# Kernel tuning notes

Hardware: AMD Instinct MI355X
Metric: run time of the kernel (lower is better)

## Reference

```python
import jax, jax.numpy as jnp
import numpy as np

GRID_MIN, GRID_MAX = -3.0, 3.0
N_AXIS = 64            # 64x64 grid -> m = 4096
LENGTHSCALE = 0.5      # RBF kernel lengthscale
EPS = 1e-6


def make_grid():
    lin = jnp.linspace(GRID_MIN, GRID_MAX, N_AXIS, dtype=jnp.float32)
    gx, gy = jnp.meshgrid(lin, lin, indexing='ij')
    return jnp.stack([gx.ravel(), gy.ravel()], axis=-1)  # [m, 2]


def setup_inputs() -> dict:
    key = jax.random.key(0)
    k1, k2 = jax.random.split(key)
    X = jax.random.normal(k1, (16, 1024, 2), dtype=jnp.float32)  # context locations
    Y = jax.random.normal(k2, (16, 1024, 8), dtype=jnp.float32)  # context values
    return {"X": X, "Y": Y}


def reference(X, Y):
    grid = make_grid()                                   # [m, 2]
    # expand_with_ones: prepend a ones channel (density channel)
    ones = jnp.ones(Y.shape[:-1] + (1,), dtype=Y.dtype)
    Yb = jnp.concatenate([ones, Y], axis=-1)             # [b, n, 1+dy]

    # kernel_smooth: RBF kernel between grid and X, contracted with Yb.
    # squared distances via the expanded form (avoids [b,m,n,2] intermediate)
    g2 = jnp.sum(grid * grid, axis=-1)                   # [m]
    x2 = jnp.sum(X * X, axis=-1)                         # [b, n]
    gx = jnp.einsum('md,bnd->bmn', grid, X)              # [b, m, n]
    d2 = g2[None, :, None] + x2[:, None, :] - 2.0 * gx   # [b, m, n]
    K = jnp.exp(-d2 / (2.0 * LENGTHSCALE * LENGTHSCALE)) # [b, m, n]

    Y_grid = jnp.einsum('bmn,bnc->bmc', K, Yb)           # [b, m, 1+dy]

    # normalise: divide feature channels by the density channel
    density = Y_grid[:, :, :1]
    feats = Y_grid[:, :, 1:] / (density + EPS)
    Y_grid = jnp.concatenate([density, feats], axis=-1)

    return grid[None], Y_grid
```

## Files before the change

### kernel.cpp

```cpp
#include <hip/hip_runtime.h>

typedef _Float16 half8   __attribute__((ext_vector_type(8)));
typedef float    floatx4 __attribute__((ext_vector_type(4)));

#define STEP  (6.0f / 63.0f)
#define SCAL  1.69864636f

__global__ __launch_bounds__(512, 2) void rkhs_fused(
    const float* __restrict__ X,
    const float* __restrict__ Y,
    float* __restrict__ out)
{
    __shared__ __align__(16) unsigned char smem[65536];
    float2*   sX    = (float2*)smem;
    float*    sYf   = (float*)(smem + 2048);
    _Float16* sEx   = (_Float16*)(smem + 10240);
    _Float16* sYb   = (_Float16*)(smem + 12288);
    _Float16* sEy   = (_Float16*)(smem + 20480);
    floatx4*  spark = (floatx4*)smem;
    float*    sfin  = (float*)smem;

    const int b   = blockIdx.x >> 4;
    const int rw  = blockIdx.x & 15;
    const int tid = threadIdx.x;
    const int w   = tid >> 6, l = tid & 63, q = l >> 4, n = l & 15;
    const int r0  = rw * 4;

    if (b == 0) {
        const int row = r0 + (tid >> 7), rem = tid & 127;
        out[(size_t)rw * 512 + tid] = (rem & 1)
            ? (-3.0f + (float)(rem >> 1) * STEP)
            : (-3.0f + (float)row * STEP);
    }

    floatx4 acc[4][4];
#pragma unroll
    for (int rr = 0; rr < 4; ++rr)
#pragma unroll
        for (int ct = 0; ct < 4; ++ct) acc[rr][ct] = (floatx4){0.f, 0.f, 0.f, 0.f};

    for (int c = 0; c < 4; ++c) {
        const int kb = c * 256;
        __syncthreads();
        if (tid < 256)
            sX[tid] = ((const float2*)X)[b * 1024 + kb + tid];
        ((float4*)sYf)[tid] =
            ((const float4*)(Y + ((size_t)b * 1024 + kb) * 8))[tid];
        __syncthreads();

        if (tid < 128) {
            const int s_loc = tid >> 4, rr = (tid >> 2) & 3, qq = tid & 3;
            const int kk = s_loc * 32 + qq * 8;
            const float gS = SCAL * (-3.0f + (float)(r0 + rr) * STEP);
            half8 h;
#pragma unroll
            for (int j = 0; j < 8; ++j) {
                const float d = fmaf(-SCAL, sX[kk + j].x, gS);
                h[j] = (_Float16)__builtin_amdgcn_exp2f(-(d * d));
            }
            *(half8*)(sEx + (s_loc * 4 + rr) * 32 + qq * 8) = h;
        }
        {
            const int kk = w * 32 + q * 8;
            half8 h;
#pragma unroll
            for (int j = 0; j < 8; ++j) {
                float v = 0.f;
                if (n == 0)      v = 1.f;
                else if (n <= 8) v = sYf[(kk + j) * 8 + n - 1];
                h[j] = (_Float16)v;
            }
            *(half8*)(sYb + (w * 64 + l) * 8) = h;
        }
#pragma unroll
        for (int i = 0; i < 4; ++i) {
            const int u = tid + 512 * i;
            const int ll = u & 63;
            const int kk = ((u >> 8) & 7) * 32 + (ll >> 4) * 8;
            const int col = ((u >> 6) & 3) * 16 + (ll & 15);
            const float gS = SCAL * (-3.0f + (float)col * STEP);
            half8 h;
#pragma unroll
            for (int j = 0; j < 8; ++j) {
                const float d = fmaf(-SCAL, sX[kk + j].y, gS);
                h[j] = (_Float16)__builtin_amdgcn_exp2f(-(d * d));
            }
            *(half8*)(sEy + (size_t)u * 8) = h;
        }
        __syncthreads();

        {
            const half8 yb = *(const half8*)(sYb + (w * 64 + l) * 8);
            half8 bp[4];
#pragma unroll
            for (int rr = 0; rr < 4; ++rr)
                bp[rr] = (*(const half8*)(sEx + (w * 4 + rr) * 32 + q * 8)) * yb;
#pragma unroll
            for (int ct = 0; ct < 4; ++ct) {
                const half8 ey = *(const half8*)(sEy + ((w * 4 + ct) * 64 + l) * 8);
#pragma unroll
                for (int rr = 0; rr < 4; ++rr)
                    acc[rr][ct] = __builtin_amdgcn_mfma_f32_16x16x32_f16(ey, bp[rr], acc[rr][ct], 0, 0, 0);
            }
        }
    }
    __syncthreads();

#define PARKA(slot)                                                        \
    { _Pragma("unroll") for (int rr = 0; rr < 4; ++rr)                     \
      _Pragma("unroll") for (int ct = 0; ct < 4; ++ct)                     \
          spark[(slot) * 1024 + (rr * 4 + ct) * 64 + l] = acc[rr][ct]; }
#define ABSORBA(slot)                                                      \
    { _Pragma("unroll") for (int rr = 0; rr < 4; ++rr)                     \
      _Pragma("unroll") for (int ct = 0; ct < 4; ++ct)                     \
          acc[rr][ct] += spark[(slot) * 1024 + (rr * 4 + ct) * 64 + l]; }

    if (w >= 4) PARKA(w - 4)
    __syncthreads();
    if (w < 4)  ABSORBA(w)
    __syncthreads();
    if (w == 2 || w == 3) PARKA(w - 2)
    __syncthreads();
    if (w < 2)  ABSORBA(w)
    __syncthreads();
    if (w == 1) PARKA(0)
    __syncthreads();

    if (w == 0) {
        ABSORBA(0)
#pragma unroll
        for (int rr = 0; rr < 4; ++rr)
#pragma unroll
            for (int ct = 0; ct < 4; ++ct)
                if (n < 9)
#pragma unroll
                    for (int i = 0; i < 4; ++i)
                        sfin[(rr * 64 + ct * 16 + q * 4 + i) * 9 + n] = acc[rr][ct][i];
    }
#undef PARKA
#undef ABSORBA
    __syncthreads();

    const size_t obase = 8192 + ((size_t)b * 4096 + (size_t)r0 * 64) * 9;
#pragma unroll
    for (int it = 0; it < 5; ++it) {
        const int idx = it * 512 + tid;
        if (idx < 2304) {
            const int m  = idx / 9;
            const int ch = idx - m * 9;
            const float dens = sfin[m * 9];
            const float v    = sfin[idx];
            out[obase + idx] = ch ? v * __builtin_amdgcn_rcpf(dens + 1e-6f) : dens;
        }
    }
}

extern "C" void kernel_launch(void* const* d_in, const int* in_sizes, int n_in,
                              void* d_out, int out_size, void* d_ws, size_t ws_size,
                              hipStream_t stream) {
    const float* X = (const float*)d_in[0];
    const float* Y = (const float*)d_in[1];
    float* out = (float*)d_out;

    rkhs_fused<<<dim3(256), dim3(512), 0, stream>>>(X, Y, out);
}
```

Measured before the change: 65.98 us.

## Stage whole context once and compute y-exponentials in registers

Replaces the four-chunk loop, which had two barriers per chunk and staged Y and the y-axis exponential tile through shared memory, with one up-front staging step and a single barrier. Each wave now loads its Y fragments straight from global memory into registers. The x-axis exponentials for all 1024 points are precomputed into shared memory once. The y-axis exponentials are computed in registers right before each MFMA instead of being stored and reloaded from LDS. This cuts synchronization and LDS traffic, but adds register pressure and moves the exp work into the MFMA loop.

```diff
diff --git a/kernel.cpp b/kernel.cpp
--- a/kernel.cpp
+++ b/kernel.cpp
@@ -12,11 +12,8 @@
     float* __restrict__ out)
 {
     __shared__ __align__(16) unsigned char smem[65536];
-    float2*   sX    = (float2*)smem;
-    float*    sYf   = (float*)(smem + 2048);
-    _Float16* sEx   = (_Float16*)(smem + 10240);
-    _Float16* sYb   = (_Float16*)(smem + 12288);
-    _Float16* sEy   = (_Float16*)(smem + 20480);
+    float*    sXy   = (float*)smem;
+    _Float16* sEx   = (_Float16*)(smem + 4096);
     floatx4*  spark = (floatx4*)smem;
     float*    sfin  = (float*)smem;
 
@@ -26,6 +23,13 @@
     const int w   = tid >> 6, l = tid & 63, q = l >> 4, n = l & 15;
     const int r0  = rw * 4;
 
+    {
+        const float2 v0 = ((const float2*)X)[b * 1024 + 2 * tid];
+        const float2 v1 = ((const float2*)X)[b * 1024 + 2 * tid + 1];
+        sXy[2 * tid]     = SCAL * v0.y;
+        sXy[2 * tid + 1] = SCAL * v1.y;
+    }
+
     if (b == 0) {
         const int row = r0 + (tid >> 7), rem = tid & 127;
         out[(size_t)rw * 512 + tid] = (rem & 1)
@@ -33,75 +37,76 @@
             : (-3.0f + (float)row * STEP);
     }
 
+    half8 ybr[4];
+#pragma unroll
+    for (int ss = 0; ss < 4; ++ss) {
+        half8 h;
+        if (n == 0) {
+#pragma unroll
+            for (int j = 0; j < 8; ++j) h[j] = (_Float16)1.0f;
+        } else if (n <= 8) {
+            const float* yp = Y + ((size_t)(b * 1024 + (w * 4 + ss) * 32 + q * 8)) * 8 + (n - 1);
+#pragma unroll
+            for (int j = 0; j < 8; ++j) h[j] = (_Float16)yp[j * 8];
+        } else {
+#pragma unroll
+            for (int j = 0; j < 8; ++j) h[j] = (_Float16)0.0f;
+        }
+        ybr[ss] = h;
+    }
+
+    if (tid < 128) {
+        const int s = tid >> 2, rr = tid & 3;
+        const float gS = SCAL * (-3.0f + (float)(r0 + rr) * STEP);
+        const float* xp = X + (size_t)(b * 1024 + s * 32) * 2;
+#pragma unroll
+        for (int g = 0; g < 4; ++g) {
+            half8 hbuf;
+#pragma unroll
+            for (int j = 0; j < 8; ++j) {
+                const float d = fmaf(-SCAL, xp[(g * 8 + j) * 2], gS);
+                hbuf[j] = (_Float16)__builtin_amdgcn_exp2f(-(d * d));
+            }
+            *(half8*)(sEx + (s * 4 + rr) * 32 + g * 8) = hbuf;
+        }
+    }
+    __syncthreads();
+
+    float gSct[4];
+#pragma unroll
+    for (int ct = 0; ct < 4; ++ct)
+        gSct[ct] = SCAL * (-3.0f + (float)(ct * 16 + n) * STEP);
+
     floatx4 acc[4][4];
 #pragma unroll
     for (int rr = 0; rr < 4; ++rr)
 #pragma unroll
         for (int ct = 0; ct < 4; ++ct) acc[rr][ct] = (floatx4){0.f, 0.f, 0.f, 0.f};
 
-    for (int c = 0; c < 4; ++c) {
-        const int kb = c * 256;
-        __syncthreads();
-        if (tid < 256)
-            sX[tid] = ((const float2*)X)[b * 1024 + kb + tid];
-        ((float4*)sYf)[tid] =
-            ((const float4*)(Y + ((size_t)b * 1024 + kb) * 8))[tid];
-        __syncthreads();
+#pragma unroll
+    for (int ss = 0; ss < 4; ++ss) {
+        const int s   = w * 4 + ss;
+        const int k0q = s * 32 + q * 8;
+        const float4 xa = *(const float4*)(sXy + k0q);
+        const float4 xb = *(const float4*)(sXy + k0q + 4);
+        const float xk[8] = {xa.x, xa.y, xa.z, xa.w, xb.x, xb.y, xb.z, xb.w};
 
-        if (tid < 128) {
-            const int s_loc = tid >> 4, rr = (tid >> 2) & 3, qq = tid & 3;
-            const int kk = s_loc * 32 + qq * 8;
-            const float gS = SCAL * (-3.0f + (float)(r0 + rr) * STEP);
-            half8 h;
+        half8 bp[4];
+#pragma unroll
+        for (int rr = 0; rr < 4; ++rr)
+            bp[rr] = (*(const half8*)(sEx + (s * 4 + rr) * 32 + q * 8)) * ybr[ss];
+
+#pragma unroll
+        for (int ct = 0; ct < 4; ++ct) {
+            half8 ey;
 #pragma unroll
             for (int j = 0; j < 8; ++j) {
-                const float d = fmaf(-SCAL, sX[kk + j].x, gS);
-                h[j] = (_Float16)__builtin_amdgcn_exp2f(-(d * d));
+                const float d = gSct[ct] - xk[j];
+                ey[j] = (_Float16)__builtin_amdgcn_exp2f(-(d * d));
             }
-            *(half8*)(sEx + (s_loc * 4 + rr) * 32 + qq * 8) = h;
-        }
-        {
-            const int kk = w * 32 + q * 8;
-            half8 h;
-#pragma unroll
-            for (int j = 0; j < 8; ++j) {
-                float v = 0.f;
-                if (n == 0)      v = 1.f;
-                else if (n <= 8) v = sYf[(kk + j) * 8 + n - 1];
-                h[j] = (_Float16)v;
-            }
-            *(half8*)(sYb + (w * 64 + l) * 8) = h;
-        }
-#pragma unroll
-        for (int i = 0; i < 4; ++i) {
-            const int u = tid + 512 * i;
-            const int ll = u & 63;
-            const int kk = ((u >> 8) & 7) * 32 + (ll >> 4) * 8;
-            const int col = ((u >> 6) & 3) * 16 + (ll & 15);
-            const float gS = SCAL * (-3.0f + (float)col * STEP);
-            half8 h;
-#pragma unroll
-            for (int j = 0; j < 8; ++j) {
-                const float d = fmaf(-SCAL, sX[kk + j].y, gS);
-                h[j] = (_Float16)__builtin_amdgcn_exp2f(-(d * d));
-            }
-            *(half8*)(sEy + (size_t)u * 8) = h;
-        }
-        __syncthreads();
-
-        {
-            const half8 yb = *(const half8*)(sYb + (w * 64 + l) * 8);
-            half8 bp[4];
 #pragma unroll
             for (int rr = 0; rr < 4; ++rr)
-                bp[rr] = (*(const half8*)(sEx + (w * 4 + rr) * 32 + q * 8)) * yb;
-#pragma unroll
-            for (int ct = 0; ct < 4; ++ct) {
-                const half8 ey = *(const half8*)(sEy + ((w * 4 + ct) * 64 + l) * 8);
-#pragma unroll
-                for (int rr = 0; rr < 4; ++rr)
-                    acc[rr][ct] = __builtin_amdgcn_mfma_f32_16x16x32_f16(ey, bp[rr], acc[rr][ct], 0, 0, 0);
-            }
+                acc[rr][ct] = __builtin_amdgcn_mfma_f32_16x16x32_f16(ey, bp[rr], acc[rr][ct], 0, 0, 0);
         }
     }
     __syncthreads();
@@ -161,6 +166,7 @@
     const float* X = (const float*)d_in[0];
     const float* Y = (const float*)d_in[1];
     float* out = (float*)d_out;
+    (void)d_ws; (void)ws_size;
 
     rkhs_fused<<<dim3(256), dim3(512), 0, stream>>>(X, Y, out);
 }
```

New measurement: 62.70 us. 5.0% less time.
